# Performance work log

Hardware: AMD Instinct MI355X
Metric: run time of the kernel (lower is better)

Reference implementation:

```python
import jax, jax.numpy as jnp
import numpy as np

D = 512          # d_model
DS = 32          # d_state
EXPAND = 2
HEADDIM = 64
R = 4            # mimo_rank
DIN = EXPAND * D             # 1024 inner dim
H = DIN // HEADDIM           # 16 heads
DFF = ((int(D * 8 / 3) + 7) // 8) * 8  # 1368 SwiGLU hidden
CHUNK = max(1, 64 // R)      # 16
BATCH, SEQ = 4, 512


def setup_inputs() -> dict:
    key = jax.random.key(0)
    ks = jax.random.split(key, 12)
    def w(k, shape, fan):
        return jax.random.normal(k, shape, jnp.float32) / np.float32(np.sqrt(fan))
    return {
        "x": jax.random.normal(ks[0], (BATCH, SEQ, D), jnp.float32),
        "mask": jnp.ones((BATCH, SEQ), jnp.float32),
        "norm1_w": jnp.ones((D,), jnp.float32),
        "norm2_w": jnp.ones((D,), jnp.float32),
        "Wz": w(ks[1], (D, DIN), D),
        "Wx": w(ks[2], (D, DIN), D),
        "Wb": w(ks[3], (D, H * R * DS), D),
        "Wc": w(ks[4], (D, H * R * DS), D),
        "Wdt": w(ks[5], (D, H), D),
        "dt_bias": jnp.zeros((H,), jnp.float32),
        "A_log": jnp.log(jnp.arange(1, H + 1, dtype=jnp.float32)),
        "D_skip": jnp.ones((H,), jnp.float32),
        "Wout": w(ks[6], (DIN, D), DIN),
        "w1": w(ks[7], (D, DFF), D),
        "w2": w(ks[8], (DFF, D), DFF),
        "w3": w(ks[9], (D, DFF), D),
    }


def rmsnorm(x, wgt, eps=1e-6):
    rms = jnp.sqrt(jnp.mean(x * x, axis=-1, keepdims=True) + eps)
    return x / rms * wgt


def ssm_mixer(x, Wz, Wx, Wb, Wc, Wdt, dt_bias, A_log, D_skip, Wout):
    # x: [B, S, D] (already masked)
    B, S, _ = x.shape
    pad = (CHUNK - S % CHUNK) % CHUNK
    if pad > 0:
        x = jnp.pad(x, ((0, 0), (0, pad), (0, 0)))
    Sp = x.shape[1]
    z = x @ Wz                                        # [B,Sp,DIN] gate
    u = (x @ Wx).reshape(B, Sp, H, HEADDIM)           # [B,Sp,H,P]
    Bm = (x @ Wb).reshape(B, Sp, H, R, DS)            # [B,Sp,H,R,N]
    Cm = (x @ Wc).reshape(B, Sp, H, R, DS)
    dt = jax.nn.softplus(x @ Wdt + dt_bias)           # [B,Sp,H]
    a = jnp.exp(dt * (-jnp.exp(A_log)))               # per-step decay [B,Sp,H]
    ud = u * dt[..., None]                            # discretized input

    def step(h, inp):
        a_t, B_t, C_t, ud_t = inp                     # [B,H], [B,H,R,N], [B,H,R,N], [B,H,P]
        h = a_t[:, :, None, None, None] * h + jnp.einsum('bhrn,bhp->bhrnp', B_t, ud_t)
        y = jnp.einsum('bhrn,bhrnp->bhp', C_t, h)
        return h, y

    h0 = jnp.zeros((B, H, R, DS, HEADDIM), x.dtype)
    xs = (a.swapaxes(0, 1), Bm.swapaxes(0, 1), Cm.swapaxes(0, 1), ud.swapaxes(0, 1))
    _, ys = jax.lax.scan(step, h0, xs)                # ys: [Sp,B,H,P]
    y = ys.swapaxes(0, 1) + u * D_skip[None, None, :, None]
    y = y.reshape(B, Sp, DIN) * jax.nn.silu(z)
    y = y @ Wout                                      # [B,Sp,D]
    return y[:, :S]


def reference(x, mask, norm1_w, norm2_w, Wz, Wx, Wb, Wc, Wdt, dt_bias,
              A_log, D_skip, Wout, w1, w2, w3):
    m = mask[..., None]
    xn = rmsnorm(x, norm1_w) * m
    y = ssm_mixer(xn, Wz, Wx, Wb, Wc, Wdt, dt_bias, A_log, D_skip, Wout) * m
    x = x + y
    xn2 = rmsnorm(x, norm2_w)
    x = x + (jax.nn.silu(xn2 @ w1) * (xn2 @ w3)) @ w2
    return x * m
```

## Files before the change

### kernel.cpp

```cpp
#include <hip/hip_runtime.h>
#include <hip/hip_bf16.h>
#include <math.h>

#define Bn 4
#define Sn 512
#define Dn 512
#define DINn 1024
#define Hn 16
#define Pn 64
#define RNn 128
#define DFFn 1368
#define KP2 1408
#define BSn (Bn*Sn)
#define CH 64
#define NCH (Sn/CH)
#define PSTR 6144
#define FSTR 2736
#define FPAD 2816

typedef __attribute__((ext_vector_type(8))) short short8;
typedef __attribute__((ext_vector_type(4))) float f32x4;

static __device__ __forceinline__ float bf2f(__hip_bfloat16 v){return __bfloat162float(v);}
static __device__ __forceinline__ __hip_bfloat16 f2bf(float v){return __float2bfloat16(v);}
static __device__ __forceinline__ short f2bfs(float v){ __hip_bfloat16 b=f2bf(v); short s; __builtin_memcpy(&s,&b,2); return s; }
static __device__ __forceinline__ float bfs2f(short s){ __hip_bfloat16 b; __builtin_memcpy(&b,&s,2); return bf2f(b); }

struct T8 {
  const float* src[8];
  __hip_bfloat16* dst[8];
  int Rr[8], Cc[8], RrPad[8], CcPad[8], gw[8];
  int start[9];
};

__global__ void transpose8_kernel(T8 d) {
  int bid = blockIdx.x;
  int i = 0;
#pragma unroll
  for (int k = 1; k < 8; ++k) if (bid >= d.start[k]) i = k;
  int rel = bid - d.start[i];
  int gx = rel % d.gw[i], gy = rel / d.gw[i];
  const float* __restrict__ in = d.src[i];
  __hip_bfloat16* __restrict__ out = d.dst[i];
  int Rr = d.Rr[i], Cc = d.Cc[i], RrPad = d.RrPad[i], CcPad = d.CcPad[i];
  __shared__ float tile[32][33];
  int c0 = gx * 32, r0 = gy * 32;
  int tx = threadIdx.x, ty = threadIdx.y;
  for (int k = ty; k < 32; k += 8) {
    int r = r0 + k, cc = c0 + tx;
    tile[k][tx] = (r < Rr && cc < Cc) ? in[(size_t)r * Cc + cc] : 0.f;
  }
  __syncthreads();
  for (int k = ty; k < 32; k += 8) {
    int r = c0 + k, cc = r0 + tx;
    if (r < CcPad && cc < RrPad) out[(size_t)r * RrPad + cc] = f2bf(tile[tx][k]);
  }
}

__global__ void rmsnorm1_dt_kernel(const float* __restrict__ x,
                                   const float* __restrict__ w,
                                   const float* __restrict__ mask,
                                   const float* __restrict__ Wdt,
                                   const float* __restrict__ dtb,
                                   const float* __restrict__ Alog,
                                   __hip_bfloat16* __restrict__ outb,
                                   float* __restrict__ dt, float* __restrict__ la) {
  __shared__ float xs[Dn];
  __shared__ float red[4];
  int row = blockIdx.x, t = threadIdx.x;
  const float* xr = x + (size_t)row * Dn;
  float v0 = xr[t], v1 = xr[t + 256];
  float ss = v0 * v0 + v1 * v1;
#pragma unroll
  for (int o = 32; o > 0; o >>= 1) ss += __shfl_down(ss, o);
  if ((t & 63) == 0) red[t >> 6] = ss;
  __syncthreads();
  float tot = red[0] + red[1] + red[2] + red[3];
  float sc = rsqrtf(tot * (1.f / Dn) + 1e-6f) * mask[row];
  float o0 = v0 * sc * w[t], o1v = v1 * sc * w[t + 256];
  outb[(size_t)row * Dn + t] = f2bf(o0);
  outb[(size_t)row * Dn + t + 256] = f2bf(o1v);
  xs[t] = o0;
  xs[t + 256] = o1v;
  __syncthreads();
  int h = t >> 4, j = t & 15;
  float s = 0.f;
  for (int k = j * 32; k < j * 32 + 32; ++k) s = fmaf(xs[k], Wdt[k * Hn + h], s);
#pragma unroll
  for (int o = 8; o > 0; o >>= 1) s += __shfl_down(s, o, 16);
  if (j == 0) {
    float v = s + dtb[h];
    float sp = (v > 20.f) ? v : log1pf(expf(v));
    float Ah = expf(Alog[h]);
    dt[(size_t)row * Hn + h] = sp;
    la[(size_t)row * Hn + h] = -Ah * sp;
  }
}

__global__ void rmsnorm2_kernel(const float* __restrict__ x,
                                const float* __restrict__ w,
                                __hip_bfloat16* __restrict__ out) {
  int row = blockIdx.x, t = threadIdx.x;
  const float* xr = x + (size_t)row * Dn;
  float v0 = xr[t], v1 = xr[t + 256];
  float ss = v0 * v0 + v1 * v1;
#pragma unroll
  for (int o = 32; o > 0; o >>= 1) ss += __shfl_down(ss, o);
  __shared__ float red[4];
  if ((t & 63) == 0) red[t >> 6] = ss;
  __syncthreads();
  float tot = red[0] + red[1] + red[2] + red[3];
  float sc = rsqrtf(tot * (1.f / Dn) + 1e-6f);
  out[(size_t)row * Dn + t] = f2bf(v0 * sc * w[t]);
  out[(size_t)row * Dn + t + 256] = f2bf(v1 * sc * w[t + 256]);
}

__global__ __launch_bounds__(256) void gemm_kernel(
    const __hip_bfloat16* __restrict__ A, const __hip_bfloat16* __restrict__ BT,
    __hip_bfloat16* __restrict__ C, int M, int N, int K) {
  __shared__ short As[2][128][40];
  __shared__ short Bs[2][128][40];
  int m0 = blockIdx.x * 128, n0 = blockIdx.y * 128;
  int t = threadIdx.x;
  int lane = t & 63, wv = t >> 6;
  int wm = (wv & 1) * 64, wn = (wv >> 1) * 64;
  f32x4 acc[4][4];
#pragma unroll
  for (int i = 0; i < 4; ++i)
#pragma unroll
    for (int j = 0; j < 4; ++j) acc[i][j] = (f32x4){0.f, 0.f, 0.f, 0.f};
  const short* Ag = (const short*)A;
  const short* Bg = (const short*)BT;
  int sr = t >> 2;
  int sc = (t & 3) * 8;
  int rb0 = n0 + sr, rb1 = n0 + sr + 64;
  bool bv0 = rb0 < N, bv1 = rb1 < N;
  const short* Ap0 = Ag + (size_t)(m0 + sr) * K + sc;
  const short* Ap1 = Ag + (size_t)(m0 + sr + 64) * K + sc;
  const short* Bp0 = Bg + (size_t)rb0 * K + sc;
  const short* Bp1 = Bg + (size_t)rb1 * K + sc;
  int kTiles = (K + 31) >> 5;
  int fr = lane & 15, fq = (lane >> 4) * 8;
  short8 a0A = 0, a1A = 0, b0A = 0, b1A = 0;
  short8 a0B = 0, a1B = 0, b0B = 0, b1B = 0;
  auto loadA = [&](int k0) {
    a0A = *(const short8*)(Ap0 + k0);
    a1A = *(const short8*)(Ap1 + k0);
    b0A = bv0 ? *(const short8*)(Bp0 + k0) : (short8)0;
    b1A = bv1 ? *(const short8*)(Bp1 + k0) : (short8)0;
  };
  auto loadB = [&](int k0) {
    a0B = *(const short8*)(Ap0 + k0);
    a1B = *(const short8*)(Ap1 + k0);
    b0B = bv0 ? *(const short8*)(Bp0 + k0) : (short8)0;
    b1B = bv1 ? *(const short8*)(Bp1 + k0) : (short8)0;
  };
  auto storeA = [&](int buf) {
    *(short8*)&As[buf][sr][sc] = a0A;
    *(short8*)&As[buf][sr + 64][sc] = a1A;
    *(short8*)&Bs[buf][sr][sc] = b0A;
    *(short8*)&Bs[buf][sr + 64][sc] = b1A;
  };
  auto storeB = [&](int buf) {
    *(short8*)&As[buf][sr][sc] = a0B;
    *(short8*)&As[buf][sr + 64][sc] = a1B;
    *(short8*)&Bs[buf][sr][sc] = b0B;
    *(short8*)&Bs[buf][sr + 64][sc] = b1B;
  };
  auto mfma = [&](int buf) {
    short8 af[4], bfr[4];
#pragma unroll
    for (int i = 0; i < 4; ++i) af[i] = *(const short8*)&As[buf][wm + i * 16 + fr][fq];
#pragma unroll
    for (int i = 0; i < 4; ++i) bfr[i] = *(const short8*)&Bs[buf][wn + i * 16 + fr][fq];
#pragma unroll
    for (int mi = 0; mi < 4; ++mi)
#pragma unroll
      for (int ni = 0; ni < 4; ++ni)
        acc[mi][ni] = __builtin_amdgcn_mfma_f32_16x16x32_bf16(af[mi], bfr[ni], acc[mi][ni], 0, 0, 0);
  };
  loadA(0);
  storeA(0);
  loadA(32);
  __syncthreads();
  for (int kt = 0; kt < kTiles; kt += 2) {
    storeA(1);
    if (kt + 2 < kTiles) loadB((kt + 2) << 5);
    mfma(0);
    __syncthreads();
    if (kt + 2 < kTiles) storeB(0);
    if (kt + 3 < kTiles) loadA((kt + 3) << 5);
    mfma(1);
    __syncthreads();
  }
  int fq4 = (lane >> 4) * 4;
#pragma unroll
  for (int mi = 0; mi < 4; ++mi)
#pragma unroll
    for (int ni = 0; ni < 4; ++ni) {
      int col = n0 + wn + ni * 16 + fr;
      if (col < N) {
        int rowb = m0 + wm + mi * 16 + fq4;
#pragma unroll
        for (int r = 0; r < 4; ++r)
          C[(size_t)(rowb + r) * N + col] = f2bf(acc[mi][ni][r]);
      }
    }
}

template <int MODE>
__global__ __launch_bounds__(256) void gemm64_ep_kernel(
    const __hip_bfloat16* __restrict__ A, const __hip_bfloat16* __restrict__ BT,
    const float* __restrict__ aux, const float* __restrict__ mask,
    float* __restrict__ out, int M, int N, int K) {
  __shared__ short As[2][64][72];
  __shared__ short Bs[2][64][72];
  int m0 = blockIdx.x * 64, n0 = blockIdx.y * 64;
  int t = threadIdx.x;
  int lane = t & 63, wv = t >> 6;
  int wm = (wv & 1) * 32, wn = (wv >> 1) * 32;
  f32x4 acc[2][2];
#pragma unroll
  for (int i = 0; i < 2; ++i)
#pragma unroll
    for (int j = 0; j < 2; ++j) acc[i][j] = (f32x4){0.f, 0.f, 0.f, 0.f};
  const short* Ag = (const short*)A;
  const short* Bg = (const short*)BT;
  int sr = t >> 2;
  int sc = (t & 3) * 16;
  const short* Ap = Ag + (size_t)(m0 + sr) * K + sc;
  const short* Bp = Bg + (size_t)(n0 + sr) * K + sc;
  int fr = lane & 15, fq = (lane >> 4) * 8;
  int kTiles = K >> 6;
  short8 a0A = 0, a1A = 0, b0A = 0, b1A = 0;
  short8 a0B = 0, a1B = 0, b0B = 0, b1B = 0;
  auto loadA = [&](int k0) {
    a0A = *(const short8*)(Ap + k0);
    a1A = *(const short8*)(Ap + k0 + 8);
    b0A = *(const short8*)(Bp + k0);
    b1A = *(const short8*)(Bp + k0 + 8);
  };
  auto loadB = [&](int k0) {
    a0B = *(const short8*)(Ap + k0);
    a1B = *(const short8*)(Ap + k0 + 8);
    b0B = *(const short8*)(Bp + k0);
    b1B = *(const short8*)(Bp + k0 + 8);
  };
  auto storeA = [&](int buf) {
    *(short8*)&As[buf][sr][sc] = a0A;
    *(short8*)&As[buf][sr][sc + 8] = a1A;
    *(short8*)&Bs[buf][sr][sc] = b0A;
    *(short8*)&Bs[buf][sr][sc + 8] = b1A;
  };
  auto storeB = [&](int buf) {
    *(short8*)&As[buf][sr][sc] = a0B;
    *(short8*)&As[buf][sr][sc + 8] = a1B;
    *(short8*)&Bs[buf][sr][sc] = b0B;
    *(short8*)&Bs[buf][sr][sc + 8] = b1B;
  };
  auto mfma = [&](int buf) {
#pragma unroll
    for (int kk = 0; kk < 2; ++kk) {
      short8 af[2], bfr[2];
#pragma unroll
      for (int i = 0; i < 2; ++i) af[i] = *(const short8*)&As[buf][wm + i * 16 + fr][kk * 32 + fq];
#pragma unroll
      for (int i = 0; i < 2; ++i) bfr[i] = *(const short8*)&Bs[buf][wn + i * 16 + fr][kk * 32 + fq];
#pragma unroll
      for (int mi = 0; mi < 2; ++mi)
#pragma unroll
        for (int ni = 0; ni < 2; ++ni)
          acc[mi][ni] = __builtin_amdgcn_mfma_f32_16x16x32_bf16(af[mi], bfr[ni], acc[mi][ni], 0, 0, 0);
    }
  };
  loadA(0);
  storeA(0);
  loadA(64);
  __syncthreads();
  for (int kt = 0; kt < kTiles; kt += 2) {
    storeA(1);
    if (kt + 2 < kTiles) loadB((kt + 2) << 6);
    mfma(0);
    __syncthreads();
    if (kt + 2 < kTiles) storeB(0);
    if (kt + 3 < kTiles) loadA((kt + 3) << 6);
    mfma(1);
    __syncthreads();
  }
  int fq4 = (lane >> 4) * 4;
#pragma unroll
  for (int mi = 0; mi < 2; ++mi)
#pragma unroll
    for (int ni = 0; ni < 2; ++ni) {
      int col = n0 + wn + ni * 16 + fr;
#pragma unroll
      for (int r = 0; r < 4; ++r) {
        int row = m0 + wm + mi * 16 + fq4 + r;
        float m = mask[row];
        size_t a = (size_t)row * N + col;
        float v = acc[mi][ni][r];
        if (MODE == 1) out[a] = aux[a] + v * m;
        else           out[a] = (aux[a] + v) * m;
      }
    }
}

__global__ __launch_bounds__(256) void gemm64g_kernel(
    const __hip_bfloat16* __restrict__ A, const __hip_bfloat16* __restrict__ BT,
    __hip_bfloat16* __restrict__ G, int M, int K) {
  __shared__ short As[2][64][72];
  __shared__ short B1s[2][64][72];
  __shared__ short B3s[2][64][72];
  int m0 = blockIdx.x * 64, n0 = blockIdx.y * 64;
  int t = threadIdx.x;
  int lane = t & 63, wv = t >> 6;
  int wm = (wv & 1) * 32, wn = (wv >> 1) * 32;
  f32x4 acc1[2][2], acc3[2][2];
#pragma unroll
  for (int i = 0; i < 2; ++i)
#pragma unroll
    for (int j = 0; j < 2; ++j) {
      acc1[i][j] = (f32x4){0.f, 0.f, 0.f, 0.f};
      acc3[i][j] = (f32x4){0.f, 0.f, 0.f, 0.f};
    }
  const short* Ag = (const short*)A;
  const short* Bg = (const short*)BT;
  int sr = t >> 2;
  int sc = (t & 3) * 16;
  const short* Ap  = Ag + (size_t)(m0 + sr) * K + sc;
  const short* B1p = Bg + (size_t)(n0 + sr) * K + sc;
  const short* B3p = Bg + (size_t)(DFFn + n0 + sr) * K + sc;
  int fr = lane & 15, fq = (lane >> 4) * 8;
  int kTiles = K >> 6;
  short8 a0A = 0, a1A = 0, c0A = 0, c1A = 0, d0A = 0, d1A = 0;
  short8 a0B = 0, a1B = 0, c0B = 0, c1B = 0, d0B = 0, d1B = 0;
  auto loadA = [&](int k0) {
    a0A = *(const short8*)(Ap + k0);
    a1A = *(const short8*)(Ap + k0 + 8);
    c0A = *(const short8*)(B1p + k0);
    c1A = *(const short8*)(B1p + k0 + 8);
    d0A = *(const short8*)(B3p + k0);
    d1A = *(const short8*)(B3p + k0 + 8);
  };
  auto loadB = [&](int k0) {
    a0B = *(const short8*)(Ap + k0);
    a1B = *(const short8*)(Ap + k0 + 8);
    c0B = *(const short8*)(B1p + k0);
    c1B = *(const short8*)(B1p + k0 + 8);
    d0B = *(const short8*)(B3p + k0);
    d1B = *(const short8*)(B3p + k0 + 8);
  };
  auto storeA = [&](int buf) {
    *(short8*)&As[buf][sr][sc] = a0A;
    *(short8*)&As[buf][sr][sc + 8] = a1A;
    *(short8*)&B1s[buf][sr][sc] = c0A;
    *(short8*)&B1s[buf][sr][sc + 8] = c1A;
    *(short8*)&B3s[buf][sr][sc] = d0A;
    *(short8*)&B3s[buf][sr][sc + 8] = d1A;
  };
  auto storeB = [&](int buf) {
    *(short8*)&As[buf][sr][sc] = a0B;
    *(short8*)&As[buf][sr][sc + 8] = a1B;
    *(short8*)&B1s[buf][sr][sc] = c0B;
    *(short8*)&B1s[buf][sr][sc + 8] = c1B;
    *(short8*)&B3s[buf][sr][sc] = d0B;
    *(short8*)&B3s[buf][sr][sc + 8] = d1B;
  };
  auto mfma = [&](int buf) {
#pragma unroll
    for (int kk = 0; kk < 2; ++kk) {
      short8 af[2], b1f[2], b3f[2];
#pragma unroll
      for (int i = 0; i < 2; ++i) af[i]  = *(const short8*)&As[buf][wm + i * 16 + fr][kk * 32 + fq];
#pragma unroll
      for (int i = 0; i < 2; ++i) b1f[i] = *(const short8*)&B1s[buf][wn + i * 16 + fr][kk * 32 + fq];
#pragma unroll
      for (int i = 0; i < 2; ++i) b3f[i] = *(const short8*)&B3s[buf][wn + i * 16 + fr][kk * 32 + fq];
#pragma unroll
      for (int mi = 0; mi < 2; ++mi)
#pragma unroll
        for (int ni = 0; ni < 2; ++ni) {
          acc1[mi][ni] = __builtin_amdgcn_mfma_f32_16x16x32_bf16(af[mi], b1f[ni], acc1[mi][ni], 0, 0, 0);
          acc3[mi][ni] = __builtin_amdgcn_mfma_f32_16x16x32_bf16(af[mi], b3f[ni], acc3[mi][ni], 0, 0, 0);
        }
    }
  };
  loadA(0);
  storeA(0);
  loadA(64);
  __syncthreads();
  for (int kt = 0; kt < kTiles; kt += 2) {
    storeA(1);
    if (kt + 2 < kTiles) loadB((kt + 2) << 6);
    mfma(0);
    __syncthreads();
    if (kt + 2 < kTiles) storeB(0);
    if (kt + 3 < kTiles) loadA((kt + 3) << 6);
    mfma(1);
    __syncthreads();
  }
  int fq4 = (lane >> 4) * 4;
#pragma unroll
  for (int mi = 0; mi < 2; ++mi)
#pragma unroll
    for (int ni = 0; ni < 2; ++ni) {
      int col = n0 + wn + ni * 16 + fr;
      bool valid = col < DFFn;
#pragma unroll
      for (int r = 0; r < 4; ++r) {
        int row = m0 + wm + mi * 16 + fq4 + r;
        float h1v = acc1[mi][ni][r];
        float sil = h1v / (1.f + __expf(-h1v));
        float g = sil * acc3[mi][ni][r];
        G[(size_t)row * KP2 + col] = valid ? f2bf(g) : f2bf(0.f);
      }
    }
}

__global__ __launch_bounds__(256) void chunk_intra_kernel(
    const __hip_bfloat16* __restrict__ P, const float* __restrict__ dt,
    const float* __restrict__ la, float* __restrict__ ys,
    float* __restrict__ Sbuf, float* __restrict__ ecL, float* __restrict__ ec) {
  int id = blockIdx.x;
  int h = id & 15, c = (id >> 4) & 7, b = id >> 7;
  int t = threadIdx.x, lane = t & 63, wv = t >> 6;
  __shared__ __align__(16) char smem[55040];
  short* sCB = (short*)smem;
  short* sB  = (short*)(smem + 18432);
  short* sUD = (short*)(smem + 35840);
  short* sG  = (short*)(smem + 45056);
  float* scum = (float*)(smem + 54272);
  float* sws  = scum + 64;
  float* sdt  = sws + 64;
  int row0 = b * Sn + c * CH;
  const short* Pb = (const short*)P;
#pragma unroll
  for (int i = 0; i < 4; ++i) {
    int idx = t + i * 256;
    int r = idx >> 4, kk = (idx & 15) * 8;
    *(short8*)&sCB[r * 136 + kk] = *(const short8*)(Pb + (size_t)(row0 + r) * PSTR + 4096 + h * 128 + kk);
    *(short8*)&sB [r * 136 + kk] = *(const short8*)(Pb + (size_t)(row0 + r) * PSTR + 2048 + h * 128 + kk);
  }
  if (t < 64) { sdt[t] = dt[(size_t)(row0 + t) * Hn + h]; scum[t] = la[(size_t)(row0 + t) * Hn + h]; }
  __syncthreads();
  if (wv == 0) {
    float v = scum[lane];
#pragma unroll
    for (int o = 1; o < 64; o <<= 1) { float n = __shfl_up(v, o); if (lane >= o) v += n; }
    scum[lane] = v;
    float c63 = __shfl(v, 63);
    sws[lane] = __expf(c63 - v);
    ec[((size_t)((b * NCH + c) * Hn + h)) * 64 + lane] = __expf(v);
    if (lane == 0) ecL[(b * NCH + c) * Hn + h] = __expf(c63);
  }
#pragma unroll
  for (int i = 0; i < 2; ++i) {
    int idx = t + i * 256;
    int s = idx >> 3, pc = (idx & 7) * 8;
    short8 uv = *(const short8*)(Pb + (size_t)(row0 + s) * PSTR + 1024 + h * 64 + pc);
    float dv = sdt[s];
#pragma unroll
    for (int j = 0; j < 8; ++j) sUD[(pc + j) * 72 + s] = f2bfs(bfs2f(uv[j]) * dv);
  }
  __syncthreads();
  int fr = lane & 15, fq = (lane >> 4) * 8, q4 = (lane >> 4) * 4;
  {
    short8 af[4];
#pragma unroll
    for (int k = 0; k < 4; ++k) af[k] = *(short8*)&sCB[(16 * wv + fr) * 136 + k * 32 + fq];
#pragma unroll
    for (int j = 0; j < 4; ++j) {
      f32x4 acc = (f32x4){0.f, 0.f, 0.f, 0.f};
#pragma unroll
      for (int k = 0; k < 4; ++k) {
        short8 bf = *(short8*)&sB[(16 * j + fr) * 136 + k * 32 + fq];
        acc = __builtin_amdgcn_mfma_f32_16x16x32_bf16(af[k], bf, acc, 0, 0, 0);
      }
      int ss = 16 * j + fr;
      float cs = scum[ss];
#pragma unroll
      for (int r = 0; r < 4; ++r) {
        int tt = 16 * wv + q4 + r;
        float w = (ss <= tt) ? __expf(scum[tt] - cs) : 0.f;
        sG[tt * 72 + ss] = f2bfs(acc[r] * w);
      }
    }
  }
  __syncthreads();
#pragma unroll
  for (int i = 0; i < 32; ++i) {
    int idx = t + i * 256;
    int rn = idx >> 6, s = idx & 63;
    sCB[rn * 72 + s] = f2bfs(bfs2f(sB[s * 136 + rn]) * sws[s]);
  }
  __syncthreads();
  {
    short8 ag[2];
#pragma unroll
    for (int k = 0; k < 2; ++k) ag[k] = *(short8*)&sG[(16 * wv + fr) * 72 + k * 32 + fq];
#pragma unroll
    for (int j = 0; j < 4; ++j) {
      f32x4 acc = (f32x4){0.f, 0.f, 0.f, 0.f};
#pragma unroll
      for (int k = 0; k < 2; ++k) {
        short8 bf = *(short8*)&sUD[(16 * j + fr) * 72 + k * 32 + fq];
        acc = __builtin_amdgcn_mfma_f32_16x16x32_bf16(ag[k], bf, acc, 0, 0, 0);
      }
#pragma unroll
      for (int r = 0; r < 4; ++r)
        ys[(size_t)(row0 + 16 * wv + q4 + r) * DINn + h * 64 + 16 * j + fr] = acc[r];
    }
  }
#pragma unroll
  for (int mt0 = 0; mt0 < 2; ++mt0) {
    int mt = wv * 2 + mt0;
    short8 ab[2];
#pragma unroll
    for (int k = 0; k < 2; ++k) ab[k] = *(short8*)&sCB[(16 * mt + fr) * 72 + k * 32 + fq];
#pragma unroll
    for (int j = 0; j < 4; ++j) {
      f32x4 acc = (f32x4){0.f, 0.f, 0.f, 0.f};
#pragma unroll
      for (int k = 0; k < 2; ++k) {
        short8 bf = *(short8*)&sUD[(16 * j + fr) * 72 + k * 32 + fq];
        acc = __builtin_amdgcn_mfma_f32_16x16x32_bf16(ab[k], bf, acc, 0, 0, 0);
      }
#pragma unroll
      for (int r = 0; r < 4; ++r)
        Sbuf[((size_t)((b * NCH + c) * Hn + h) * RNn + 16 * mt + q4 + r) * 64 + 16 * j + fr] = acc[r];
    }
  }
}

__global__ void chunk_state_kernel(const float* __restrict__ Sbuf, const float* __restrict__ ecL,
                                   float* __restrict__ Hp) {
  int bh = blockIdx.x >> 5;
  int j = (blockIdx.x & 31) * 256 + threadIdx.x;
  int b = bh >> 4, h = bh & 15;
  float hp = 0.f;
#pragma unroll
  for (int c = 0; c < NCH; ++c) {
    size_t addr = ((size_t)((b * NCH + c) * Hn + h)) * 8192 + j;
    Hp[addr] = hp;
    hp = ecL[(b * NCH + c) * Hn + h] * hp + Sbuf[addr];
  }
}

__global__ __launch_bounds__(256) void inter_gate_kernel(
    const __hip_bfloat16* __restrict__ P, const float* __restrict__ Hp,
    const float* __restrict__ ec, const float* __restrict__ ys,
    const float* __restrict__ Dsk, __hip_bfloat16* __restrict__ y2b) {
  int id = blockIdx.x;
  int h = id & 15, c = (id >> 4) & 7, b = id >> 7;
  int t = threadIdx.x, lane = t & 63, wv = t >> 6;
  __shared__ __align__(16) short sC[64 * 136];
  __shared__ __align__(16) short sHt[64 * 136];
  __shared__ __align__(16) short sz[64 * 64];
  __shared__ __align__(16) short su[64 * 64];
  __shared__ float sec[64];
  int row0 = b * Sn + c * CH;
  const short* Pb = (const short*)P;
#pragma unroll
  for (int i = 0; i < 2; ++i) {
    int idx = t + i * 256;
    int r = idx >> 3, pc = (idx & 7) * 8;
    *(short8*)&sz[r * 64 + pc] = *(const short8*)(Pb + (size_t)(row0 + r) * PSTR + h * 64 + pc);
    *(short8*)&su[r * 64 + pc] = *(const short8*)(Pb + (size_t)(row0 + r) * PSTR + 1024 + h * 64 + pc);
  }
  if (c > 0) {
    size_t hbase = ((size_t)((b * NCH + c) * Hn + h)) * 8192;
#pragma unroll
    for (int i = 0; i < 4; ++i) {
      int idx = t + i * 256;
      int r = idx >> 4, kk = (idx & 15) * 8;
      *(short8*)&sC[r * 136 + kk] = *(const short8*)(Pb + (size_t)(row0 + r) * PSTR + 4096 + h * 128 + kk);
    }
#pragma unroll
    for (int i = 0; i < 32; ++i) {
      int idx = t + i * 256;
      int rn = idx >> 6, p = idx & 63;
      sHt[p * 136 + rn] = f2bfs(Hp[hbase + idx]);
    }
    if (t < 64) sec[t] = ec[((size_t)((b * NCH + c) * Hn + h)) * 64 + t];
  }
  __syncthreads();
  int fr = lane & 15, fq = (lane >> 4) * 8, q4 = (lane >> 4) * 4;
  f32x4 acc[4];
#pragma unroll
  for (int j = 0; j < 4; ++j) acc[j] = (f32x4){0.f, 0.f, 0.f, 0.f};
  if (c > 0) {
    short8 af[4];
#pragma unroll
    for (int k = 0; k < 4; ++k) af[k] = *(short8*)&sC[(16 * wv + fr) * 136 + k * 32 + fq];
#pragma unroll
    for (int j = 0; j < 4; ++j)
#pragma unroll
      for (int k = 0; k < 4; ++k) {
        short8 bf = *(short8*)&sHt[(16 * j + fr) * 136 + k * 32 + fq];
        acc[j] = __builtin_amdgcn_mfma_f32_16x16x32_bf16(af[k], bf, acc[j], 0, 0, 0);
      }
  }
  float dsk = Dsk[h];
#pragma unroll
  for (int j = 0; j < 4; ++j) {
    int col = 16 * j + fr;
#pragma unroll
    for (int r = 0; r < 4; ++r) {
      int tt = 16 * wv + q4 + r;
      size_t a = (size_t)(row0 + tt) * DINn + h * 64 + col;
      float val = ys[a];
      if (c > 0) val += sec[tt] * acc[j][r];
      float uu = bfs2f(su[tt * 64 + col]);
      float zz = bfs2f(sz[tt * 64 + col]);
      float sil = zz / (1.f + __expf(-zz));
      y2b[a] = f2bf((val + uu * dsk) * sil);
    }
  }
}

extern "C" void kernel_launch(void* const* d_in, const int* in_sizes, int n_in,
                              void* d_out, int out_size, void* d_ws, size_t ws_size,
                              hipStream_t stream) {
  const float* x    = (const float*)d_in[0];
  const float* mask = (const float*)d_in[1];
  const float* n1w  = (const float*)d_in[2];
  const float* n2w  = (const float*)d_in[3];
  const float* Wz   = (const float*)d_in[4];
  const float* Wx   = (const float*)d_in[5];
  const float* Wb   = (const float*)d_in[6];
  const float* Wc   = (const float*)d_in[7];
  const float* Wdt  = (const float*)d_in[8];
  const float* dtb  = (const float*)d_in[9];
  const float* Alog = (const float*)d_in[10];
  const float* Dsk  = (const float*)d_in[11];
  const float* Wout = (const float*)d_in[12];
  const float* w1   = (const float*)d_in[13];
  const float* w2   = (const float*)d_in[14];
  const float* w3   = (const float*)d_in[15];

  char* ws = (char*)d_ws;
  size_t off = 0;
  auto alloc = [&](size_t bytes) {
    char* p = ws + off;
    off += (bytes + 255) & ~(size_t)255;
    return p;
  };
  __hip_bfloat16* xnb = (__hip_bfloat16*)alloc((size_t)BSn * Dn * 2);
  __hip_bfloat16* P = (__hip_bfloat16*)alloc((size_t)BSn * PSTR * 2);
  float* dt  = (float*)alloc((size_t)BSn * Hn * 4);
  float* la  = (float*)alloc((size_t)BSn * Hn * 4);
  float* ys  = (float*)alloc((size_t)BSn * DINn * 4);
  float* ecL = (float*)alloc((size_t)Bn * NCH * Hn * 4);
  float* ec  = (float*)alloc((size_t)Bn * NCH * Hn * 64 * 4);
  __hip_bfloat16* WallT = (__hip_bfloat16*)alloc((size_t)PSTR * Dn * 2);
  __hip_bfloat16* WoutT = (__hip_bfloat16*)alloc((size_t)Dn * DINn * 2);
  __hip_bfloat16* w13T  = (__hip_bfloat16*)alloc((size_t)FPAD * Dn * 2);
  __hip_bfloat16* w2T   = (__hip_bfloat16*)alloc((size_t)Dn * KP2 * 2);
  char* arena = alloc(34000000);
  float* Sbuf = (float*)arena;
  float* Hp   = (float*)(arena + 16777216);
  __hip_bfloat16* y2b = (__hip_bfloat16*)arena;
  float* xres = (float*)(arena + 8388608);
  __hip_bfloat16* gatedb = (__hip_bfloat16*)(arena + 16777216);

  T8 td;
  td.src[0] = Wz;   td.dst[0] = WallT;                      td.Rr[0] = 512;  td.Cc[0] = 1024; td.RrPad[0] = 512;  td.CcPad[0] = 1024;
  td.src[1] = Wx;   td.dst[1] = WallT + (size_t)1024 * 512; td.Rr[1] = 512;  td.Cc[1] = 1024; td.RrPad[1] = 512;  td.CcPad[1] = 1024;
  td.src[2] = Wb;   td.dst[2] = WallT + (size_t)2048 * 512; td.Rr[2] = 512;  td.Cc[2] = 2048; td.RrPad[2] = 512;  td.CcPad[2] = 2048;
  td.src[3] = Wc;   td.dst[3] = WallT + (size_t)4096 * 512; td.Rr[3] = 512;  td.Cc[3] = 2048; td.RrPad[3] = 512;  td.CcPad[3] = 2048;
  td.src[4] = Wout; td.dst[4] = WoutT;                      td.Rr[4] = 1024; td.Cc[4] = 512;  td.RrPad[4] = 1024; td.CcPad[4] = 512;
  td.src[5] = w1;   td.dst[5] = w13T;                       td.Rr[5] = 512;  td.Cc[5] = 1368; td.RrPad[5] = 512;  td.CcPad[5] = 1368;
  td.src[6] = w3;   td.dst[6] = w13T + (size_t)1368 * 512;  td.Rr[6] = 512;  td.Cc[6] = 1368; td.RrPad[6] = 512;  td.CcPad[6] = 1448;
  td.src[7] = w2;   td.dst[7] = w2T;                        td.Rr[7] = 1368; td.Cc[7] = 512;  td.RrPad[7] = KP2;  td.CcPad[7] = 512;
  int tot = 0;
  for (int i = 0; i < 8; ++i) {
    td.gw[i] = (td.CcPad[i] + 31) / 32;
    int gh = (td.RrPad[i] + 31) / 32;
    td.start[i] = tot;
    tot += td.gw[i] * gh;
  }
  td.start[8] = tot;

  transpose8_kernel<<<tot, dim3(32, 8), 0, stream>>>(td);
  rmsnorm1_dt_kernel<<<BSn, 256, 0, stream>>>(x, n1w, mask, Wdt, dtb, Alog, xnb, dt, la);
  gemm_kernel<<<dim3(16, 48), 256, 0, stream>>>(xnb, WallT, P, BSn, PSTR, Dn);
  chunk_intra_kernel<<<Bn * NCH * Hn, 256, 0, stream>>>(P, dt, la, ys, Sbuf, ecL, ec);
  chunk_state_kernel<<<Bn * Hn * 32, 256, 0, stream>>>(Sbuf, ecL, Hp);
  inter_gate_kernel<<<Bn * NCH * Hn, 256, 0, stream>>>(P, Hp, ec, ys, Dsk, y2b);
  gemm64_ep_kernel<1><<<dim3(32, 8), 256, 0, stream>>>(y2b, WoutT, x, mask, xres, BSn, Dn, DINn);
  rmsnorm2_kernel<<<BSn, 256, 0, stream>>>(xres, n2w, xnb);
  gemm64g_kernel<<<dim3(32, KP2 / 64), 256, 0, stream>>>(xnb, w13T, gatedb, BSn, Dn);
  gemm64_ep_kernel<2><<<dim3(32, 8), 256, 0, stream>>>(gatedb, w2T, xres, mask, (float*)d_out, BSn, Dn, KP2);
}
```

Baseline: 219.7 us.

## Store SSM intermediates in bf16 and fuse transpose with rmsnorm prep

Switches the intra-chunk outputs ys, the chunk states Sbuf, and the propagated states Hp from fp32 to bf16 storage. This halves the intermediate traffic between chunk_intra, chunk_state and inter_gate, and the workspace arena is remapped to match. The weight transpose and the rmsnorm1/dt kernels are merged into a single launch that dispatches on block index, saving one kernel launch. The cost is extra rounding on the recurrent state and the intra-chunk output, which may lose accuracy.

```diff
diff --git a/kernel.cpp b/kernel.cpp
--- a/kernel.cpp
+++ b/kernel.cpp
@@ -33,67 +33,65 @@
   int start[9];
 };
 
-__global__ void transpose8_kernel(T8 d) {
-  int bid = blockIdx.x;
-  int i = 0;
-#pragma unroll
-  for (int k = 1; k < 8; ++k) if (bid >= d.start[k]) i = k;
-  int rel = bid - d.start[i];
-  int gx = rel % d.gw[i], gy = rel / d.gw[i];
-  const float* __restrict__ in = d.src[i];
-  __hip_bfloat16* __restrict__ out = d.dst[i];
-  int Rr = d.Rr[i], Cc = d.Cc[i], RrPad = d.RrPad[i], CcPad = d.CcPad[i];
+__global__ __launch_bounds__(256) void prep_kernel(
+    T8 d, const float* __restrict__ x, const float* __restrict__ w,
+    const float* __restrict__ mask, const float* __restrict__ Wdt,
+    const float* __restrict__ dtb, const float* __restrict__ Alog,
+    __hip_bfloat16* __restrict__ outb, float* __restrict__ dt,
+    float* __restrict__ la, int tstart) {
   __shared__ float tile[32][33];
-  int c0 = gx * 32, r0 = gy * 32;
-  int tx = threadIdx.x, ty = threadIdx.y;
-  for (int k = ty; k < 32; k += 8) {
-    int r = r0 + k, cc = c0 + tx;
-    tile[k][tx] = (r < Rr && cc < Cc) ? in[(size_t)r * Cc + cc] : 0.f;
-  }
-  __syncthreads();
-  for (int k = ty; k < 32; k += 8) {
-    int r = c0 + k, cc = r0 + tx;
-    if (r < CcPad && cc < RrPad) out[(size_t)r * RrPad + cc] = f2bf(tile[tx][k]);
-  }
-}
-
-__global__ void rmsnorm1_dt_kernel(const float* __restrict__ x,
-                                   const float* __restrict__ w,
-                                   const float* __restrict__ mask,
-                                   const float* __restrict__ Wdt,
-                                   const float* __restrict__ dtb,
-                                   const float* __restrict__ Alog,
-                                   __hip_bfloat16* __restrict__ outb,
-                                   float* __restrict__ dt, float* __restrict__ la) {
   __shared__ float xs[Dn];
   __shared__ float red[4];
-  int row = blockIdx.x, t = threadIdx.x;
-  const float* xr = x + (size_t)row * Dn;
-  float v0 = xr[t], v1 = xr[t + 256];
-  float ss = v0 * v0 + v1 * v1;
-#pragma unroll
-  for (int o = 32; o > 0; o >>= 1) ss += __shfl_down(ss, o);
-  if ((t & 63) == 0) red[t >> 6] = ss;
-  __syncthreads();
-  float tot = red[0] + red[1] + red[2] + red[3];
-  float sc = rsqrtf(tot * (1.f / Dn) + 1e-6f) * mask[row];
-  float o0 = v0 * sc * w[t], o1v = v1 * sc * w[t + 256];
-  outb[(size_t)row * Dn + t] = f2bf(o0);
-  outb[(size_t)row * Dn + t + 256] = f2bf(o1v);
-  xs[t] = o0;
-  xs[t + 256] = o1v;
-  __syncthreads();
-  int h = t >> 4, j = t & 15;
-  float s = 0.f;
-  for (int k = j * 32; k < j * 32 + 32; ++k) s = fmaf(xs[k], Wdt[k * Hn + h], s);
-#pragma unroll
-  for (int o = 8; o > 0; o >>= 1) s += __shfl_down(s, o, 16);
-  if (j == 0) {
-    float v = s + dtb[h];
-    float sp = (v > 20.f) ? v : log1pf(expf(v));
-    float Ah = expf(Alog[h]);
-    dt[(size_t)row * Hn + h] = sp;
-    la[(size_t)row * Hn + h] = -Ah * sp;
+  int bid = blockIdx.x, t = threadIdx.x;
+  if (bid < tstart) {
+    int i = 0;
+#pragma unroll
+    for (int k = 1; k < 8; ++k) if (bid >= d.start[k]) i = k;
+    int rel = bid - d.start[i];
+    int gx = rel % d.gw[i], gy = rel / d.gw[i];
+    const float* in = d.src[i];
+    __hip_bfloat16* out = d.dst[i];
+    int Rr = d.Rr[i], Cc = d.Cc[i], RrPad = d.RrPad[i], CcPad = d.CcPad[i];
+    int c0 = gx * 32, r0 = gy * 32;
+    int tx = t & 31, ty = t >> 5;
+    for (int k = ty; k < 32; k += 8) {
+      int r = r0 + k, cc = c0 + tx;
+      tile[k][tx] = (r < Rr && cc < Cc) ? in[(size_t)r * Cc + cc] : 0.f;
+    }
+    __syncthreads();
+    for (int k = ty; k < 32; k += 8) {
+      int r = c0 + k, cc = r0 + tx;
+      if (r < CcPad && cc < RrPad) out[(size_t)r * RrPad + cc] = f2bf(tile[tx][k]);
+    }
+  } else {
+    int row = bid - tstart;
+    const float* xr = x + (size_t)row * Dn;
+    float v0 = xr[t], v1 = xr[t + 256];
+    float ss = v0 * v0 + v1 * v1;
+#pragma unroll
+    for (int o = 32; o > 0; o >>= 1) ss += __shfl_down(ss, o);
+    if ((t & 63) == 0) red[t >> 6] = ss;
+    __syncthreads();
+    float tot = red[0] + red[1] + red[2] + red[3];
+    float sc = rsqrtf(tot * (1.f / Dn) + 1e-6f) * mask[row];
+    float o0 = v0 * sc * w[t], o1v = v1 * sc * w[t + 256];
+    outb[(size_t)row * Dn + t] = f2bf(o0);
+    outb[(size_t)row * Dn + t + 256] = f2bf(o1v);
+    xs[t] = o0;
+    xs[t + 256] = o1v;
+    __syncthreads();
+    int h = t >> 4, j = t & 15;
+    float s = 0.f;
+    for (int k = j * 32; k < j * 32 + 32; ++k) s = fmaf(xs[k], Wdt[k * Hn + h], s);
+#pragma unroll
+    for (int o = 8; o > 0; o >>= 1) s += __shfl_down(s, o, 16);
+    if (j == 0) {
+      float v = s + dtb[h];
+      float sp = (v > 20.f) ? v : log1pf(expf(v));
+      float Ah = expf(Alog[h]);
+      dt[(size_t)row * Hn + h] = sp;
+      la[(size_t)row * Hn + h] = -Ah * sp;
+    }
   }
 }
 
@@ -419,8 +417,8 @@
 
 __global__ __launch_bounds__(256) void chunk_intra_kernel(
     const __hip_bfloat16* __restrict__ P, const float* __restrict__ dt,
-    const float* __restrict__ la, float* __restrict__ ys,
-    float* __restrict__ Sbuf, float* __restrict__ ecL, float* __restrict__ ec) {
+    const float* __restrict__ la, __hip_bfloat16* __restrict__ ysb,
+    __hip_bfloat16* __restrict__ Sbuf, float* __restrict__ ecL, float* __restrict__ ec) {
   int id = blockIdx.x;
   int h = id & 15, c = (id >> 4) & 7, b = id >> 7;
   int t = threadIdx.x, lane = t & 63, wv = t >> 6;
@@ -508,7 +506,7 @@
       }
 #pragma unroll
       for (int r = 0; r < 4; ++r)
-        ys[(size_t)(row0 + 16 * wv + q4 + r) * DINn + h * 64 + 16 * j + fr] = acc[r];
+        ysb[(size_t)(row0 + 16 * wv + q4 + r) * DINn + h * 64 + 16 * j + fr] = f2bf(acc[r]);
     }
   }
 #pragma unroll
@@ -527,28 +525,35 @@
       }
 #pragma unroll
       for (int r = 0; r < 4; ++r)
-        Sbuf[((size_t)((b * NCH + c) * Hn + h) * RNn + 16 * mt + q4 + r) * 64 + 16 * j + fr] = acc[r];
-    }
-  }
-}
-
-__global__ void chunk_state_kernel(const float* __restrict__ Sbuf, const float* __restrict__ ecL,
-                                   float* __restrict__ Hp) {
-  int bh = blockIdx.x >> 5;
-  int j = (blockIdx.x & 31) * 256 + threadIdx.x;
+        ((short*)Sbuf)[((size_t)((b * NCH + c) * Hn + h) * RNn + 16 * mt + q4 + r) * 64 + 16 * j + fr] =
+            f2bfs(acc[r]);
+    }
+  }
+}
+
+__global__ void chunk_state_kernel(const __hip_bfloat16* __restrict__ Sbuf,
+                                   const float* __restrict__ ecL,
+                                   __hip_bfloat16* __restrict__ Hp) {
+  int bh = blockIdx.x >> 4;
+  int j = ((blockIdx.x & 15) * 256 + threadIdx.x) * 2;
   int b = bh >> 4, h = bh & 15;
-  float hp = 0.f;
+  const short* Sb = (const short*)Sbuf;
+  short* Hs = (short*)Hp;
+  float hp0 = 0.f, hp1 = 0.f;
 #pragma unroll
   for (int c = 0; c < NCH; ++c) {
     size_t addr = ((size_t)((b * NCH + c) * Hn + h)) * 8192 + j;
-    Hp[addr] = hp;
-    hp = ecL[(b * NCH + c) * Hn + h] * hp + Sbuf[addr];
+    short2 sv = *(const short2*)(Sb + addr);
+    *(short2*)(Hs + addr) = make_short2(f2bfs(hp0), f2bfs(hp1));
+    float e = ecL[(b * NCH + c) * Hn + h];
+    hp0 = e * hp0 + bfs2f(sv.x);
+    hp1 = e * hp1 + bfs2f(sv.y);
   }
 }
 
 __global__ __launch_bounds__(256) void inter_gate_kernel(
-    const __hip_bfloat16* __restrict__ P, const float* __restrict__ Hp,
-    const float* __restrict__ ec, const float* __restrict__ ys,
+    const __hip_bfloat16* __restrict__ P, const __hip_bfloat16* __restrict__ Hp,
+    const float* __restrict__ ec, const __hip_bfloat16* __restrict__ ysb,
     const float* __restrict__ Dsk, __hip_bfloat16* __restrict__ y2b) {
   int id = blockIdx.x;
   int h = id & 15, c = (id >> 4) & 7, b = id >> 7;
@@ -568,6 +573,7 @@
     *(short8*)&su[r * 64 + pc] = *(const short8*)(Pb + (size_t)(row0 + r) * PSTR + 1024 + h * 64 + pc);
   }
   if (c > 0) {
+    const short* Hps = (const short*)Hp;
     size_t hbase = ((size_t)((b * NCH + c) * Hn + h)) * 8192;
 #pragma unroll
     for (int i = 0; i < 4; ++i) {
@@ -579,7 +585,7 @@
     for (int i = 0; i < 32; ++i) {
       int idx = t + i * 256;
       int rn = idx >> 6, p = idx & 63;
-      sHt[p * 136 + rn] = f2bfs(Hp[hbase + idx]);
+      sHt[p * 136 + rn] = Hps[hbase + idx];
     }
     if (t < 64) sec[t] = ec[((size_t)((b * NCH + c) * Hn + h)) * 64 + t];
   }
@@ -608,7 +614,7 @@
     for (int r = 0; r < 4; ++r) {
       int tt = 16 * wv + q4 + r;
       size_t a = (size_t)(row0 + tt) * DINn + h * 64 + col;
-      float val = ys[a];
+      float val = bf2f(ysb[a]);
       if (c > 0) val += sec[tt] * acc[j][r];
       float uu = bfs2f(su[tt * 64 + col]);
       float zz = bfs2f(sz[tt * 64 + col]);
@@ -649,19 +655,19 @@
   __hip_bfloat16* P = (__hip_bfloat16*)alloc((size_t)BSn * PSTR * 2);
   float* dt  = (float*)alloc((size_t)BSn * Hn * 4);
   float* la  = (float*)alloc((size_t)BSn * Hn * 4);
-  float* ys  = (float*)alloc((size_t)BSn * DINn * 4);
+  __hip_bfloat16* ysb = (__hip_bfloat16*)alloc((size_t)BSn * DINn * 2);
   float* ecL = (float*)alloc((size_t)Bn * NCH * Hn * 4);
   float* ec  = (float*)alloc((size_t)Bn * NCH * Hn * 64 * 4);
   __hip_bfloat16* WallT = (__hip_bfloat16*)alloc((size_t)PSTR * Dn * 2);
   __hip_bfloat16* WoutT = (__hip_bfloat16*)alloc((size_t)Dn * DINn * 2);
   __hip_bfloat16* w13T  = (__hip_bfloat16*)alloc((size_t)FPAD * Dn * 2);
   __hip_bfloat16* w2T   = (__hip_bfloat16*)alloc((size_t)Dn * KP2 * 2);
-  char* arena = alloc(34000000);
-  float* Sbuf = (float*)arena;
-  float* Hp   = (float*)(arena + 16777216);
-  __hip_bfloat16* y2b = (__hip_bfloat16*)arena;
-  float* xres = (float*)(arena + 8388608);
-  __hip_bfloat16* gatedb = (__hip_bfloat16*)(arena + 16777216);
+  char* arena = alloc(22000000);
+  __hip_bfloat16* Sbuf = (__hip_bfloat16*)arena;
+  __hip_bfloat16* Hp   = (__hip_bfloat16*)(arena + 8388608);
+  __hip_bfloat16* y2b  = (__hip_bfloat16*)(arena + 16777216);
+  float* xres          = (float*)arena;
+  __hip_bfloat16* gatedb = (__hip_bfloat16*)(arena + 4194304);
 
   T8 td;
   td.src[0] = Wz;   td.dst[0] = WallT;                      td.Rr[0] = 512;  td.Cc[0] = 1024; td.RrPad[0] = 512;  td.CcPad[0] = 1024;
@@ -681,12 +687,11 @@
   }
   td.start[8] = tot;
 
-  transpose8_kernel<<<tot, dim3(32, 8), 0, stream>>>(td);
-  rmsnorm1_dt_kernel<<<BSn, 256, 0, stream>>>(x, n1w, mask, Wdt, dtb, Alog, xnb, dt, la);
+  prep_kernel<<<tot + BSn, 256, 0, stream>>>(td, x, n1w, mask, Wdt, dtb, Alog, xnb, dt, la, tot);
   gemm_kernel<<<dim3(16, 48), 256, 0, stream>>>(xnb, WallT, P, BSn, PSTR, Dn);
-  chunk_intra_kernel<<<Bn * NCH * Hn, 256, 0, stream>>>(P, dt, la, ys, Sbuf, ecL, ec);
-  chunk_state_kernel<<<Bn * Hn * 32, 256, 0, stream>>>(Sbuf, ecL, Hp);
-  inter_gate_kernel<<<Bn * NCH * Hn, 256, 0, stream>>>(P, Hp, ec, ys, Dsk, y2b);
+  chunk_intra_kernel<<<Bn * NCH * Hn, 256, 0, stream>>>(P, dt, la, ysb, Sbuf, ecL, ec);
+  chunk_state_kernel<<<Bn * Hn * 16, 256, 0, stream>>>(Sbuf, ecL, Hp);
+  inter_gate_kernel<<<Bn * NCH * Hn, 256, 0, stream>>>(P, Hp, ec, ysb, Dsk, y2b);
   gemm64_ep_kernel<1><<<dim3(32, 8), 256, 0, stream>>>(y2b, WoutT, x, mask, xres, BSn, Dn, DINn);
   rmsnorm2_kernel<<<BSn, 256, 0, stream>>>(xres, n2w, xnb);
   gemm64g_kernel<<<dim3(32, KP2 / 64), 256, 0, stream>>>(xnb, w13T, gatedb, BSn, Dn);
```

Measured after the change: 214.7 us. 1.02x faster.
